# Kernel optimization log

Measured on AMD Instinct MI355X. Metric: run time of the kernel, lower is better.

Reference implementation:

```python
import jax, jax.numpy as jnp
import numpy as np

H, KD, VD = 8, 64, 64
W = 1.25  # custom weight scale


def layer_norm(x, g, b, eps=1e-5):
    m = x.mean(-1, keepdims=True)
    v = ((x - m) ** 2).mean(-1, keepdims=True)
    return (x - m) * jax.lax.rsqrt(v + eps) * g + b


def cross_attention(x1, x2, wq, wk, wv, wo, bo, wm):
    # Conv1d kernel_size=1 == matmul; channel axis splits as (heads, dim)
    b, s1, _ = x1.shape
    s2 = x2.shape[1]
    q = (x1 @ wq.T).reshape(b, s1, H, KD).transpose(0, 2, 1, 3)  # bhqk
    k = (x2 @ wk.T).reshape(b, s2, H, KD).transpose(0, 2, 1, 3)
    v = (x2 @ wv.T).reshape(b, s2, H, VD).transpose(0, 2, 1, 3)
    attn = jnp.einsum('bhqd,bhsd->bhqs', q, k) * (1.0 / (KD ** 0.5))
    attn = jax.nn.softmax(attn * wm, axis=-1)  # elementwise weight BEFORE softmax
    o = jnp.einsum('bhqs,bhsv->bhqv', attn, v)
    o = o.transpose(0, 2, 1, 3).reshape(b, s1, H * VD)
    return o @ wo.T + bo


def make_wm1(nvars, sl2, patch_num):
    sl = sl2 // 2
    wm = jnp.ones((nvars, sl2), jnp.float32)
    wm = wm.at[:2 * patch_num, :sl].multiply(W)
    wm = wm.at[2 * patch_num:, sl:].multiply(W)
    return wm[None, None]  # broadcast over batch, heads


def make_wm2(nvars, sv, patch_num, patch_num_v):
    wm = jnp.ones((nvars, sv), jnp.float32)
    wm = wm.at[:patch_num, :patch_num_v].multiply(W)
    wm = wm.at[patch_num:2 * patch_num, patch_num_v:2 * patch_num_v].multiply(W)
    wm = wm.at[2 * patch_num:, 2 * patch_num_v:].multiply(W)
    return wm[None, None]


def forward(cords_features, spatial_features, speed_features,
            wq1, wk1, wv1, wo1, bo1, wq2, wk2, wv2, wo2, bo2,
            ln1_g, ln1_b, ln2_g, ln2_b, ln3_g, ln3_b,
            ffn_w1, ffn_b1, ffn_w2, ffn_b2):
    b, nvars, d = cords_features.shape
    patch_num = nvars // 3
    patch_num_v = speed_features.shape[1] // 3
    wm1 = make_wm1(nvars, spatial_features.shape[1], patch_num)
    wm2 = make_wm2(nvars, 3 * patch_num_v, patch_num, patch_num_v)
    x = cross_attention(cords_features, spatial_features, wq1, wk1, wv1, wo1, bo1, wm1)
    x = layer_norm(x + cords_features, ln1_g, ln1_b)
    r2 = x
    x = cross_attention(x, speed_features, wq2, wk2, wv2, wo2, bo2, wm2)
    x = layer_norm(x + r2, ln2_g, ln2_b)
    r3 = x
    h = jax.nn.gelu(x @ ffn_w1.T + ffn_b1, approximate=False)
    x = h @ ffn_w2.T + ffn_b2
    return layer_norm(x + r3, ln3_g, ln3_b)


def setup_inputs():
    key = jax.random.key(0)
    ks = jax.random.split(key, 16)
    D, DF = 512, 2048
    s = 0.02
    inp = {
        'cords_features': jax.random.normal(ks[0], (8, 768, D), jnp.float32),
        'spatial_features': jax.random.normal(ks[1], (8, 1024, D), jnp.float32),
        'speed_features': jax.random.normal(ks[2], (8, 768, D), jnp.float32),
        'wq1': jax.random.normal(ks[3], (H * KD, D)) * s,
        'wk1': jax.random.normal(ks[4], (H * KD, D)) * s,
        'wv1': jax.random.normal(ks[5], (H * VD, D)) * s,
        'wo1': jax.random.normal(ks[6], (D, H * VD)) * s,
        'bo1': jnp.zeros((D,), jnp.float32),
        'wq2': jax.random.normal(ks[7], (H * KD, D)) * s,
        'wk2': jax.random.normal(ks[8], (H * KD, D)) * s,
        'wv2': jax.random.normal(ks[9], (H * VD, D)) * s,
        'wo2': jax.random.normal(ks[10], (D, H * VD)) * s,
        'bo2': jnp.zeros((D,), jnp.float32),
        'ln1_g': jnp.ones((D,), jnp.float32), 'ln1_b': jnp.zeros((D,), jnp.float32),
        'ln2_g': jnp.ones((D,), jnp.float32), 'ln2_b': jnp.zeros((D,), jnp.float32),
        'ln3_g': jnp.ones((D,), jnp.float32), 'ln3_b': jnp.zeros((D,), jnp.float32),
        'ffn_w1': jax.random.normal(ks[11], (DF, D)) * s,
        'ffn_b1': jnp.zeros((DF,), jnp.float32),
        'ffn_w2': jax.random.normal(ks[12], (D, DF)) * s,
        'ffn_b2': jnp.zeros((D,), jnp.float32),
    }
    return inp


def reference(cords_features, spatial_features, speed_features,
              wq1, wk1, wv1, wo1, bo1, wq2, wk2, wv2, wo2, bo2,
              ln1_g, ln1_b, ln2_g, ln2_b, ln3_g, ln3_b,
              ffn_w1, ffn_b1, ffn_w2, ffn_b2):
    return forward(cords_features, spatial_features, speed_features,
                   wq1, wk1, wv1, wo1, bo1, wq2, wk2, wv2, wo2, bo2,
                   ln1_g, ln1_b, ln2_g, ln2_b, ln3_g, ln3_b,
                   ffn_w1, ffn_b1, ffn_w2, ffn_b2)
```

## Files before the change

### kernel.cpp

```cpp
#include <hip/hip_runtime.h>
#include <hip/hip_bf16.h>


#define LN_EPS 1e-5f
#define WSCALE 1.25f

typedef __attribute__((ext_vector_type(8))) short short8;
typedef __attribute__((ext_vector_type(4))) float floatx4;
typedef unsigned short us;

__device__ __forceinline__ float bf2f(us u) {
    union { unsigned int i; float f; } v; v.i = ((unsigned int)u) << 16; return v.f;
}
__device__ __forceinline__ us f2bf(float f) {
    union { float f; unsigned int i; } v; v.f = f;
    return (us)((v.i + 0x7FFFu + ((v.i >> 16) & 1u)) >> 16);
}
__device__ __forceinline__ float gelu_f(float v) {
    float x  = v * 0.70710678118654752f;
    float ax = fabsf(x);
    float t  = 1.0f / (1.0f + 0.3275911f * ax);
    float p  = t * (0.254829592f + t * (-0.284496736f + t * (1.421413741f +
               t * (-1.453152027f + t * 1.061405429f))));
    float er = 1.0f - p * __expf(-ax * ax);
    er = copysignf(er, x);
    return 0.5f * v * (1.0f + er);
}

struct CastArgs {
    const float* src[13];
    us* dst[13];
    int blk_ofs[14];
};
__global__ __launch_bounds__(256) void cast_all(CastArgs a)
{
    int b = blockIdx.x;
    int e = 0;
    while (b >= a.blk_ofs[e + 1]) ++e;
    int i = ((b - a.blk_ofs[e]) * 256 + threadIdx.x) * 8;
    const float* s = a.src[e];
    us* d = a.dst[e];
    float4 x = *(const float4*)(s + i);
    float4 y = *(const float4*)(s + i + 4);
    *(ushort4*)(d + i)     = make_ushort4(f2bf(x.x), f2bf(x.y), f2bf(x.z), f2bf(x.w));
    *(ushort4*)(d + i + 4) = make_ushort4(f2bf(y.x), f2bf(y.y), f2bf(y.z), f2bf(y.w));
}

__global__ __launch_bounds__(256) void gemm64(
    const us* __restrict__ A, const us* __restrict__ Bw,
    const float* __restrict__ bias, us* __restrict__ Cb,
    int M, int N, int K, int flags)
{
    __shared__ us As[2][64 * 64];
    __shared__ us Bs[2][64 * 64];

    int t = threadIdx.x;
    int wave = t >> 6, lane = t & 63;
    int m0 = blockIdx.y * 64, n0 = blockIdx.x * 64;
    int wr = (wave >> 1) * 32, wc = (wave & 1) * 32;

    int r_in = lane >> 3;
    int pq   = lane & 7;
    const us* gA[2]; const us* gB[2];
    int lofs[2];
#pragma unroll
    for (int c = 0; c < 2; ++c) {
        int r = 16 * wave + 8 * c + r_in;
        int q = pq ^ (r & 7);
        gA[c] = A  + (size_t)(m0 + r) * K + 8 * q;
        gB[c] = Bw + (size_t)(n0 + r) * K + 8 * q;
        lofs[c] = (16 * wave + 8 * c) * 64;
    }

    int fcol = lane & 15, fj = lane >> 4;
    int aoff[2][2], boff[2][2];
#pragma unroll
    for (int mt = 0; mt < 2; ++mt)
#pragma unroll
        for (int kc = 0; kc < 2; ++kc) {
            int fr = wr + 16 * mt + fcol;
            aoff[mt][kc] = fr * 64 + ((kc * 4 + fj) ^ (fr & 7)) * 8;
            int br = wc + 16 * mt + fcol;
            boff[mt][kc] = br * 64 + ((kc * 4 + fj) ^ (br & 7)) * 8;
        }

    floatx4 acc[2][2] = {};

    auto stage = [&](int buf, int k0) {
#pragma unroll
        for (int c = 0; c < 2; ++c) {
            __builtin_amdgcn_global_load_lds(
                (const __attribute__((address_space(1))) void*)(gA[c] + k0),
                (__attribute__((address_space(3))) void*)(As[buf] + lofs[c]), 16, 0, 0);
            __builtin_amdgcn_global_load_lds(
                (const __attribute__((address_space(1))) void*)(gB[c] + k0),
                (__attribute__((address_space(3))) void*)(Bs[buf] + lofs[c]), 16, 0, 0);
        }
    };

    int ktrips = K >> 6;
    stage(0, 0);
    for (int tt = 0; tt < ktrips; ++tt) {
        int buf = tt & 1;
        if (tt + 1 < ktrips) {
            stage(buf ^ 1, (tt + 1) << 6);
            asm volatile("s_waitcnt vmcnt(4)" ::: "memory");
        } else {
            asm volatile("s_waitcnt vmcnt(0)" ::: "memory");
        }
        __builtin_amdgcn_s_barrier();
        asm volatile("" ::: "memory");

        const us* as_ = As[buf];
        const us* bs_ = Bs[buf];
        short8 af[2][2], bfr[2][2];
#pragma unroll
        for (int mt = 0; mt < 2; ++mt)
#pragma unroll
            for (int kc = 0; kc < 2; ++kc) {
                af[mt][kc]  = *(const short8*)(as_ + aoff[mt][kc]);
                bfr[mt][kc] = *(const short8*)(bs_ + boff[mt][kc]);
            }
#pragma unroll
        for (int kc = 0; kc < 2; ++kc)
#pragma unroll
            for (int mt = 0; mt < 2; ++mt)
#pragma unroll
                for (int nt = 0; nt < 2; ++nt)
                    acc[mt][nt] = __builtin_amdgcn_mfma_f32_16x16x32_bf16(
                        af[mt][kc], bfr[nt][kc], acc[mt][nt], 0, 0, 0);

        asm volatile("" ::: "memory");
        __builtin_amdgcn_s_barrier();
    }

    int rq = lane >> 4;
#pragma unroll
    for (int mt = 0; mt < 2; ++mt)
#pragma unroll
        for (int nt = 0; nt < 2; ++nt) {
            int col = n0 + wc + 16 * nt + fcol;
            float bv = (flags & 1) ? bias[col] : 0.f;
#pragma unroll
            for (int r = 0; r < 4; ++r) {
                int row = m0 + wr + 16 * mt + rq * 4 + r;
                Cb[(size_t)row * N + col] = f2bf(acc[mt][nt][r] + bv);
            }
        }
}

template<int BM, int BN>
__global__ __launch_bounds__(256) void gemm_t(
    const us* __restrict__ A, const us* __restrict__ Bw,
    const float* __restrict__ bias, float* __restrict__ Cf,
    us* __restrict__ Cb, int M, int N, int K, int flags,
    int vS, us* __restrict__ Vtg)
{
    constexpr int WN = BN / 2;
    constexpr int MT = 4;
    constexpr int NT = WN / 16;
    constexpr int CA = BM / 32;
    constexpr int CB = BN / 32;

    __shared__ us As[2][BM * 64];
    __shared__ us Bs[2][BN * 64];

    int t = threadIdx.x;
    int wave = t >> 6, lane = t & 63;
    int m0 = blockIdx.y * BM, n0 = blockIdx.x * BN;
    int wr = (wave >> 1) * 64, wc = (wave & 1) * WN;

    int r_in = lane >> 3;
    int pq   = lane & 7;
    const us* gA[CA]; int lofsA[CA];
#pragma unroll
    for (int c = 0; c < CA; ++c) {
        int r = 32 * c + 8 * wave + r_in;
        int q = pq ^ (r & 7);
        gA[c] = A + (size_t)(m0 + r) * K + 8 * q;
        lofsA[c] = (32 * c + 8 * wave) * 64;
    }
    const us* gB[CB]; int lofsB[CB];
#pragma unroll
    for (int c = 0; c < CB; ++c) {
        int r = 32 * c + 8 * wave + r_in;
        int q = pq ^ (r & 7);
        gB[c] = Bw + (size_t)(n0 + r) * K + 8 * q;
        lofsB[c] = (32 * c + 8 * wave) * 64;
    }

    int fcol = lane & 15, fj = lane >> 4;
    int aoff[MT][2], boff[NT][2];
#pragma unroll
    for (int mt = 0; mt < MT; ++mt)
#pragma unroll
        for (int kc = 0; kc < 2; ++kc) {
            int fr = wr + 16 * mt + fcol;
            aoff[mt][kc] = fr * 64 + ((kc * 4 + fj) ^ (fr & 7)) * 8;
        }
#pragma unroll
    for (int nt = 0; nt < NT; ++nt)
#pragma unroll
        for (int kc = 0; kc < 2; ++kc) {
            int br = wc + 16 * nt + fcol;
            boff[nt][kc] = br * 64 + ((kc * 4 + fj) ^ (br & 7)) * 8;
        }

    floatx4 acc[MT][NT] = {};

    auto stage = [&](int buf, int k0) {
#pragma unroll
        for (int c = 0; c < CA; ++c)
            __builtin_amdgcn_global_load_lds(
                (const __attribute__((address_space(1))) void*)(gA[c] + k0),
                (__attribute__((address_space(3))) void*)(As[buf] + lofsA[c]), 16, 0, 0);
#pragma unroll
        for (int c = 0; c < CB; ++c)
            __builtin_amdgcn_global_load_lds(
                (const __attribute__((address_space(1))) void*)(gB[c] + k0),
                (__attribute__((address_space(3))) void*)(Bs[buf] + lofsB[c]), 16, 0, 0);
    };

    int ktrips = K >> 6;
    stage(0, 0);
    for (int tt = 0; tt < ktrips; ++tt) {
        int buf = tt & 1;
        if (tt + 1 < ktrips) {
            stage(buf ^ 1, (tt + 1) << 6);
            asm volatile("s_waitcnt vmcnt(8)" ::: "memory");
        } else {
            asm volatile("s_waitcnt vmcnt(0)" ::: "memory");
        }
        __builtin_amdgcn_s_barrier();
        asm volatile("" ::: "memory");

        const us* as_ = As[buf];
        const us* bs_ = Bs[buf];
        short8 af[MT][2], bfr[NT][2];
#pragma unroll
        for (int mt = 0; mt < MT; ++mt)
#pragma unroll
            for (int kc = 0; kc < 2; ++kc)
                af[mt][kc] = *(const short8*)(as_ + aoff[mt][kc]);
#pragma unroll
        for (int nt = 0; nt < NT; ++nt)
#pragma unroll
            for (int kc = 0; kc < 2; ++kc)
                bfr[nt][kc] = *(const short8*)(bs_ + boff[nt][kc]);
#pragma unroll
        for (int kc = 0; kc < 2; ++kc)
#pragma unroll
            for (int mt = 0; mt < MT; ++mt)
#pragma unroll
                for (int nt = 0; nt < NT; ++nt)
                    acc[mt][nt] = __builtin_amdgcn_mfma_f32_16x16x32_bf16(
                        af[mt][kc], bfr[nt][kc], acc[mt][nt], 0, 0, 0);

        asm volatile("" ::: "memory");
        __builtin_amdgcn_s_barrier();
    }

    int rq = lane >> 4;
    if (flags & 8) {
        int b = m0 / vS;
        int s_base = m0 - b * vS;
        if (n0 < 512) {
#pragma unroll
            for (int mt = 0; mt < MT; ++mt)
#pragma unroll
                for (int nt = 0; nt < NT; ++nt) {
                    int col = n0 + wc + 16 * nt + fcol;
#pragma unroll
                    for (int r = 0; r < 4; ++r) {
                        int rloc = wr + 16 * mt + rq * 4 + r;
                        Cb[(size_t)(m0 + rloc) * 512 + col] = f2bf(acc[mt][nt][r]);
                    }
                }
        } else {
#pragma unroll
            for (int mt = 0; mt < MT; ++mt)
#pragma unroll
                for (int nt = 0; nt < NT; ++nt) {
                    int cv = n0 + wc + 16 * nt + fcol - 512;
                    int hv = cv >> 6, dv = cv & 63;
                    int sb = s_base + wr + 16 * mt + rq * 4;
                    ushort4 pk = make_ushort4(
                        f2bf(acc[mt][nt][0]), f2bf(acc[mt][nt][1]),
                        f2bf(acc[mt][nt][2]), f2bf(acc[mt][nt][3]));
                    *(ushort4*)(Vtg + ((size_t)(b * 8 + hv) * 64 + dv) * vS + sb) = pk;
                }
        }
        return;
    }

#pragma unroll
    for (int mt = 0; mt < MT; ++mt)
#pragma unroll
        for (int nt = 0; nt < NT; ++nt) {
            int col = n0 + wc + 16 * nt + fcol;
            float bv = (flags & 1) ? bias[col] : 0.f;
#pragma unroll
            for (int r = 0; r < 4; ++r) {
                int row = m0 + wr + 16 * mt + rq * 4 + r;
                float v = acc[mt][nt][r] + bv;
                if (flags & 2) v = gelu_f(v);
                if (flags & 4) Cb[(size_t)row * N + col] = f2bf(v);
                else           Cf[(size_t)row * N + col] = v;
            }
        }
}

__global__ __launch_bounds__(256, 3) void attn_kernel(
    const us* __restrict__ Q, const us* __restrict__ Kf,
    const us* __restrict__ Vg, us* __restrict__ O,
    int S1, int S2, int shift)
{
    __shared__ us Qs[64 * 64];
    __shared__ us Ks[2][64 * 64];
    __shared__ us Vs[2][64 * 64];
    __shared__ us Ps[64 * 72];

    int t = threadIdx.x;
    int wave = t >> 6, lane = t & 63;
    int quad = lane >> 4, l15 = lane & 15;
    int q0 = blockIdx.x * 64, hh = blockIdx.y, bb = blockIdx.z;
    int qb = wave * 16;

    int r_in = lane >> 3, pq = lane & 7;
    const us *gK[2], *gV[2];
    int lofs[2];
#pragma unroll
    for (int c2 = 0; c2 < 2; ++c2) {
        int r = qb + 8 * c2 + r_in;
        int lq = pq ^ (r & 7);
        const us* gQ = Q + ((size_t)bb * S1 + q0 + r) * 512 + hh * 64 + 8 * lq;
        gK[c2] = Kf + ((size_t)bb * S2 + r) * 512 + hh * 64 + 8 * lq;
        gV[c2] = Vg + ((size_t)(bb * 8 + hh) * 64 + r) * S2 + 8 * lq;
        lofs[c2] = (qb + 8 * c2) * 64;
        __builtin_amdgcn_global_load_lds(
            (const __attribute__((address_space(1))) void*)gQ,
            (__attribute__((address_space(3))) void*)(Qs + lofs[c2]), 16, 0, 0);
    }

    int aoffQ[2], poffP[2], boff[4][2];
#pragma unroll
    for (int kc = 0; kc < 2; ++kc) {
        int ph = ((kc * 4 + quad) ^ (l15 & 7)) * 8;
        aoffQ[kc] = (qb + l15) * 64 + ph;
        poffP[kc] = (qb + l15) * 72 + ph;
#pragma unroll
        for (int nt = 0; nt < 4; ++nt)
            boff[nt][kc] = (16 * nt + l15) * 64 + ph;
    }
    int pwoff[4][4];
#pragma unroll
    for (int r = 0; r < 4; ++r) {
        int row = qb + quad * 4 + r;
#pragma unroll
        for (int nt = 0; nt < 4; ++nt) {
            int s = 16 * nt + l15;
            pwoff[nt][r] = row * 72 + (((s >> 3) ^ (row & 7)) * 8) + (s & 7);
        }
    }

    floatx4 acc_o[4] = {};
    float l_part[4] = {0.f, 0.f, 0.f, 0.f};
    int qsh[4];
#pragma unroll
    for (int r = 0; r < 4; ++r) qsh[r] = (q0 + qb + quad * 4 + r) >> shift;

    auto stageKV = [&](int buf, int cc) {
#pragma unroll
        for (int c2 = 0; c2 < 2; ++c2) {
            __builtin_amdgcn_global_load_lds(
                (const __attribute__((address_space(1))) void*)(gK[c2] + (size_t)cc * 512),
                (__attribute__((address_space(3))) void*)(Ks[buf] + lofs[c2]), 16, 0, 0);
            __builtin_amdgcn_global_load_lds(
                (const __attribute__((address_space(1))) void*)(gV[c2] + cc),
                (__attribute__((address_space(3))) void*)(Vs[buf] + lofs[c2]), 16, 0, 0);
        }
    };

    stageKV(0, 0);
    asm volatile("s_waitcnt vmcnt(4)" ::: "memory");
    __builtin_amdgcn_s_barrier();
    asm volatile("" ::: "memory");
    short8 aq0 = *(const short8*)(Qs + aoffQ[0]);
    short8 aq1 = *(const short8*)(Qs + aoffQ[1]);

    int ntile = S2 >> 6;
    for (int ti = 0; ti < ntile; ++ti) {
        int buf = ti & 1;
        if (ti + 1 < ntile) {
            stageKV(buf ^ 1, (ti + 1) << 6);
            asm volatile("s_waitcnt vmcnt(4)" ::: "memory");
        } else {
            asm volatile("s_waitcnt vmcnt(0)" ::: "memory");
        }
        __builtin_amdgcn_s_barrier();
        asm volatile("" ::: "memory");

        const us* ks_ = Ks[buf];
        const us* vs_ = Vs[buf];
        int cbase = ti << 6;

        floatx4 s_acc[4] = {};
#pragma unroll
        for (int nt = 0; nt < 4; ++nt) {
            short8 bk0 = *(const short8*)(ks_ + boff[nt][0]);
            short8 bk1 = *(const short8*)(ks_ + boff[nt][1]);
            s_acc[nt] = __builtin_amdgcn_mfma_f32_16x16x32_bf16(aq0, bk0, s_acc[nt], 0, 0, 0);
            s_acc[nt] = __builtin_amdgcn_mfma_f32_16x16x32_bf16(aq1, bk1, s_acc[nt], 0, 0, 0);
        }

#pragma unroll
        for (int nt = 0; nt < 4; ++nt) {
            int srs = (cbase + 16 * nt + l15) >> shift;
#pragma unroll
            for (int r = 0; r < 4; ++r) {
                float fct = (qsh[r] == srs) ? (0.125f * WSCALE) : 0.125f;
                float p = __expf(s_acc[nt][r] * fct);
                s_acc[nt][r] = p;
                l_part[r] += p;
            }
        }

#pragma unroll
        for (int nt = 0; nt < 4; ++nt)
#pragma unroll
            for (int r = 0; r < 4; ++r)
                Ps[pwoff[nt][r]] = f2bf(s_acc[nt][r]);
        __builtin_amdgcn_wave_barrier();

        short8 ap0 = *(const short8*)(Ps + poffP[0]);
        short8 ap1 = *(const short8*)(Ps + poffP[1]);
#pragma unroll
        for (int nt = 0; nt < 4; ++nt) {
            short8 bv0 = *(const short8*)(vs_ + boff[nt][0]);
            short8 bv1 = *(const short8*)(vs_ + boff[nt][1]);
            acc_o[nt] = __builtin_amdgcn_mfma_f32_16x16x32_bf16(ap0, bv0, acc_o[nt], 0, 0, 0);
            acc_o[nt] = __builtin_amdgcn_mfma_f32_16x16x32_bf16(ap1, bv1, acc_o[nt], 0, 0, 0);
        }

        asm volatile("" ::: "memory");
        __builtin_amdgcn_s_barrier();
    }

#pragma unroll
    for (int r = 0; r < 4; ++r) {
#pragma unroll
        for (int off = 8; off; off >>= 1)
            l_part[r] += __shfl_xor(l_part[r], off, 16);
    }
#pragma unroll
    for (int r = 0; r < 4; ++r) {
        float inv = 1.0f / l_part[r];
        size_t base = ((size_t)bb * S1 + q0 + qb + quad * 4 + r) * 512 + hh * 64;
#pragma unroll
        for (int nt = 0; nt < 4; ++nt)
            O[base + 16 * nt + l15] = f2bf(acc_o[nt][r] * inv);
    }
}

__global__ __launch_bounds__(256) void ln_kernel(
    const us* __restrict__ X, const float* __restrict__ R,
    const float* __restrict__ g, const float* __restrict__ bta,
    float* __restrict__ out, us* __restrict__ outb)
{
    int row = blockIdx.x;
    int t   = threadIdx.x;
    const us*    xr = X + (size_t)row * 512;
    const float* rr = R + (size_t)row * 512;
    float v0 = bf2f(xr[t]) + rr[t];
    float v1 = bf2f(xr[t + 256]) + rr[t + 256];
    float s  = v0 + v1;
    float sq = v0 * v0 + v1 * v1;
#pragma unroll
    for (int off = 32; off; off >>= 1) {
        s  += __shfl_xor(s, off, 64);
        sq += __shfl_xor(sq, off, 64);
    }
    __shared__ float ps[4], psq[4];
    int w = t >> 6;
    if ((t & 63) == 0) { ps[w] = s; psq[w] = sq; }
    __syncthreads();
    float S  = ps[0] + ps[1] + ps[2] + ps[3];
    float SQ = psq[0] + psq[1] + psq[2] + psq[3];
    float mean = S * (1.0f / 512.0f);
    float var  = SQ * (1.0f / 512.0f) - mean * mean;
    float inv  = rsqrtf(var + LN_EPS);
    float y0 = (v0 - mean) * inv * g[t] + bta[t];
    float y1 = (v1 - mean) * inv * g[t + 256] + bta[t + 256];
    out[(size_t)row * 512 + t]       = y0;
    out[(size_t)row * 512 + t + 256] = y1;
    if (outb) {
        outb[(size_t)row * 512 + t]       = f2bf(y0);
        outb[(size_t)row * 512 + t + 256] = f2bf(y1);
    }
}

extern "C" void kernel_launch(void* const* d_in, const int* in_sizes, int n_in,
                              void* d_out, int out_size, void* d_ws, size_t ws_size,
                              hipStream_t stream)
{
    const float* cords   = (const float*)d_in[0];
    const float* spatial = (const float*)d_in[1];
    const float* speed   = (const float*)d_in[2];
    const float* wq1 = (const float*)d_in[3];
    const float* wk1 = (const float*)d_in[4];
    const float* wv1 = (const float*)d_in[5];
    const float* wo1 = (const float*)d_in[6];
    const float* bo1 = (const float*)d_in[7];
    const float* wq2 = (const float*)d_in[8];
    const float* wk2 = (const float*)d_in[9];
    const float* wv2 = (const float*)d_in[10];
    const float* wo2 = (const float*)d_in[11];
    const float* bo2 = (const float*)d_in[12];
    const float* ln1g = (const float*)d_in[13];
    const float* ln1b = (const float*)d_in[14];
    const float* ln2g = (const float*)d_in[15];
    const float* ln2b = (const float*)d_in[16];
    const float* ln3g = (const float*)d_in[17];
    const float* ln3b = (const float*)d_in[18];
    const float* fw1 = (const float*)d_in[19];
    const float* fb1 = (const float*)d_in[20];
    const float* fw2 = (const float*)d_in[21];
    const float* fb2 = (const float*)d_in[22];

    const int B = 8, S1 = 768, S2 = 1024, Sv = 768, D = 512, DF = 2048;
    const int M1 = B * S1;
    const int M2 = B * S2;

    char* w = (char*)d_ws;
    us* q_bf = (us*)w;              w += (size_t)M1 * D * 2;
    us* k_bf = (us*)w;              w += (size_t)M2 * D * 2;
    us* vt   = (us*)w;              w += (size_t)M2 * D * 2;
    us* o_bf = (us*)w;              w += (size_t)M1 * D * 2;
    us* p_bf = (us*)w;              w += (size_t)M1 * D * 2;
    float* x1 = (float*)w;          w += (size_t)M1 * D * 4;
    us* cords_bf   = (us*)w;        w += (size_t)M1 * D * 2;
    us* spatial_bf = (us*)w;        w += (size_t)M2 * D * 2;
    us* speed_bf   = (us*)w;        w += (size_t)M1 * D * 2;
    us* wq1b = (us*)w;              w += (size_t)D * D * 2;
    us* wk1b = (us*)w;              w += (size_t)D * D * 2;
    us* wv1b = (us*)w;              w += (size_t)D * D * 2;
    us* wo1b = (us*)w;              w += (size_t)D * D * 2;
    us* wq2b = (us*)w;              w += (size_t)D * D * 2;
    us* wk2b = (us*)w;              w += (size_t)D * D * 2;
    us* wv2b = (us*)w;              w += (size_t)D * D * 2;
    us* wo2b = (us*)w;              w += (size_t)D * D * 2;
    us* fw1b = (us*)w;              w += (size_t)DF * D * 2;
    us* fw2b = (us*)w;              w += (size_t)DF * D * 2;

    us* h_bf  = q_bf;
    us* y_bf  = p_bf;
    us* x1_bf = spatial_bf;
    us* x2_bf = cords_bf;
    float* x2 = (float*)d_out;

    dim3 blk(256);

    {
        CastArgs ca;
        const float* srcs[13] = {cords, spatial, speed, wq1, wk1, wv1, wo1,
                                 wq2, wk2, wv2, wo2, fw1, fw2};
        us* dsts[13] = {cords_bf, spatial_bf, speed_bf, wq1b, wk1b, wv1b, wo1b,
                        wq2b, wk2b, wv2b, wo2b, fw1b, fw2b};
        int ns[13] = {M1 * D, M2 * D, M1 * D, D * D, D * D, D * D, D * D,
                      D * D, D * D, D * D, D * D, DF * D, DF * D};
        int ofs = 0;
        for (int i = 0; i < 13; ++i) {
            ca.src[i] = srcs[i]; ca.dst[i] = dsts[i];
            ca.blk_ofs[i] = ofs; ofs += ns[i] / 2048;
        }
        ca.blk_ofs[13] = ofs;
        cast_all<<<dim3(ofs), blk, 0, stream>>>(ca);
    }

    auto g64  = [](int M, int N) { return dim3(N / 64,  M / 64); };
    auto g128 = [](int M, int N) { return dim3(N / 128, M / 128); };

    gemm64<<<g64(M1, D), blk, 0, stream>>>(cords_bf, wq1b, nullptr, q_bf, M1, D, D, 0);
    gemm_t<128, 128><<<g128(M2, 1024), blk, 0, stream>>>(spatial_bf, wk1b, nullptr, nullptr, k_bf,
                                                         M2, 1024, D, 8, S2, vt);
    attn_kernel<<<dim3(S1 / 64, 8, B), blk, 0, stream>>>(q_bf, k_bf, vt, o_bf, S1, S2, 9);
    gemm64<<<g64(M1, D), blk, 0, stream>>>(o_bf, wo1b, bo1, p_bf, M1, D, D, 1);
    ln_kernel<<<M1, blk, 0, stream>>>(p_bf, cords, ln1g, ln1b, x1, x1_bf);

    gemm64<<<g64(M1, D), blk, 0, stream>>>(x1_bf, wq2b, nullptr, q_bf, M1, D, D, 0);
    gemm_t<128, 128><<<g128(M1, 1024), blk, 0, stream>>>(speed_bf, wk2b, nullptr, nullptr, k_bf,
                                                         M1, 1024, D, 8, Sv, vt);
    attn_kernel<<<dim3(S1 / 64, 8, B), blk, 0, stream>>>(q_bf, k_bf, vt, o_bf, S1, Sv, 8);
    gemm64<<<g64(M1, D), blk, 0, stream>>>(o_bf, wo2b, bo2, p_bf, M1, D, D, 1);
    ln_kernel<<<M1, blk, 0, stream>>>(p_bf, x1, ln2g, ln2b, x2, x2_bf);

    gemm_t<128, 128><<<g128(M1, DF), blk, 0, stream>>>(x2_bf, fw1b, fb1, nullptr, h_bf,
                                                       M1, DF, D, 1 | 2 | 4, 0, nullptr);
    gemm64<<<g64(M1, D), blk, 0, stream>>>(h_bf, fw2b, fb2, y_bf, M1, D, DF, 1);
    ln_kernel<<<M1, blk, 0, stream>>>(y_bf, x2, ln3g, ln3b, (float*)d_out, nullptr);

    (void)in_sizes; (void)n_in; (void)out_size; (void)ws_size;
}
```

Before: 357.3 us.

## Replace double-buffered GEMM with 256x128 triple-buffer ring kernel using 512 threads

Replaces the 128x128 double-buffered gemm_t with gemm_ring. It uses 256x128 tiles, 8 waves, and a 3-slot LDS ring that prefetches two K-steps ahead. Each K-step's loads are split into two phases interleaved with the two k-chunks of MFMA work, and MFMA runs under raised s_setprio. There is one barrier per iteration instead of two. The aim is to hide global-to-LDS latency and cut barrier overhead for the K/V projections and FFN1, at the cost of more LDS per block and fewer blocks in the grid.

Result: no change. 353.7 us (-1.0%).

```diff
diff --git a/kernel.cpp b/kernel.cpp
--- a/kernel.cpp
+++ b/kernel.cpp
@@ -150,114 +150,135 @@
 }
 
 template<int BM, int BN>
-__global__ __launch_bounds__(256) void gemm_t(
+__global__ __launch_bounds__(512, 2) void gemm_ring(
     const us* __restrict__ A, const us* __restrict__ Bw,
-    const float* __restrict__ bias, float* __restrict__ Cf,
-    us* __restrict__ Cb, int M, int N, int K, int flags,
-    int vS, us* __restrict__ Vtg)
+    const float* __restrict__ bias, us* __restrict__ Cb,
+    int M, int N, int K, int flags, int vS, us* __restrict__ Vtg)
 {
-    constexpr int WN = BN / 2;
-    constexpr int MT = 4;
-    constexpr int NT = WN / 16;
-    constexpr int CA = BM / 32;
-    constexpr int CB = BN / 32;
-
-    __shared__ us As[2][BM * 64];
-    __shared__ us Bs[2][BN * 64];
+    static_assert(BM == 256 && BN == 128, "gemm_ring fixed at 256x128");
+    constexpr int SLOT = (BM + BN) * 64;
+    __shared__ us L[3 * SLOT];
 
     int t = threadIdx.x;
     int wave = t >> 6, lane = t & 63;
     int m0 = blockIdx.y * BM, n0 = blockIdx.x * BN;
-    int wr = (wave >> 1) * 64, wc = (wave & 1) * WN;
-
-    int r_in = lane >> 3;
-    int pq   = lane & 7;
-    const us* gA[CA]; int lofsA[CA];
-#pragma unroll
-    for (int c = 0; c < CA; ++c) {
-        int r = 32 * c + 8 * wave + r_in;
+    int wr = (wave >> 1) * 64, wc = (wave & 1) * 64;
+
+    int r_in = lane >> 3, pq = lane & 7;
+    const us* gA[4]; int lA[4];
+#pragma unroll
+    for (int c = 0; c < 4; ++c) {
+        int r = 64 * c + 8 * wave + r_in;
         int q = pq ^ (r & 7);
         gA[c] = A + (size_t)(m0 + r) * K + 8 * q;
-        lofsA[c] = (32 * c + 8 * wave) * 64;
-    }
-    const us* gB[CB]; int lofsB[CB];
-#pragma unroll
-    for (int c = 0; c < CB; ++c) {
-        int r = 32 * c + 8 * wave + r_in;
+        lA[c] = (64 * c + 8 * wave) * 64;
+    }
+    const us* gB[2]; int lB[2];
+#pragma unroll
+    for (int c = 0; c < 2; ++c) {
+        int r = 64 * c + 8 * wave + r_in;
         int q = pq ^ (r & 7);
         gB[c] = Bw + (size_t)(n0 + r) * K + 8 * q;
-        lofsB[c] = (32 * c + 8 * wave) * 64;
+        lB[c] = BM * 64 + (64 * c + 8 * wave) * 64;
     }
 
     int fcol = lane & 15, fj = lane >> 4;
-    int aoff[MT][2], boff[NT][2];
-#pragma unroll
-    for (int mt = 0; mt < MT; ++mt)
+    int aoff[4][2], boff[4][2];
+#pragma unroll
+    for (int mt = 0; mt < 4; ++mt)
 #pragma unroll
         for (int kc = 0; kc < 2; ++kc) {
             int fr = wr + 16 * mt + fcol;
             aoff[mt][kc] = fr * 64 + ((kc * 4 + fj) ^ (fr & 7)) * 8;
         }
 #pragma unroll
-    for (int nt = 0; nt < NT; ++nt)
+    for (int nt = 0; nt < 4; ++nt)
 #pragma unroll
         for (int kc = 0; kc < 2; ++kc) {
             int br = wc + 16 * nt + fcol;
-            boff[nt][kc] = br * 64 + ((kc * 4 + fj) ^ (br & 7)) * 8;
-        }
-
-    floatx4 acc[MT][NT] = {};
-
-    auto stage = [&](int buf, int k0) {
-#pragma unroll
-        for (int c = 0; c < CA; ++c)
+            boff[nt][kc] = BM * 64 + br * 64 + ((kc * 4 + fj) ^ (br & 7)) * 8;
+        }
+
+    floatx4 acc[4][4] = {};
+
+    auto stage_p0 = [&](int slot, int kt) {
+        us* base = L + slot * SLOT;
+#pragma unroll
+        for (int c = 0; c < 3; ++c)
             __builtin_amdgcn_global_load_lds(
-                (const __attribute__((address_space(1))) void*)(gA[c] + k0),
-                (__attribute__((address_space(3))) void*)(As[buf] + lofsA[c]), 16, 0, 0);
-#pragma unroll
-        for (int c = 0; c < CB; ++c)
+                (const __attribute__((address_space(1))) void*)(gA[c] + (size_t)kt * 64),
+                (__attribute__((address_space(3))) void*)(base + lA[c]), 16, 0, 0);
+    };
+    auto stage_p1 = [&](int slot, int kt) {
+        us* base = L + slot * SLOT;
+        __builtin_amdgcn_global_load_lds(
+            (const __attribute__((address_space(1))) void*)(gA[3] + (size_t)kt * 64),
+            (__attribute__((address_space(3))) void*)(base + lA[3]), 16, 0, 0);
+#pragma unroll
+        for (int c = 0; c < 2; ++c)
             __builtin_amdgcn_global_load_lds(
-                (const __attribute__((address_space(1))) void*)(gB[c] + k0),
-                (__attribute__((address_space(3))) void*)(Bs[buf] + lofsB[c]), 16, 0, 0);
+                (const __attribute__((address_space(1))) void*)(gB[c] + (size_t)kt * 64),
+                (__attribute__((address_space(3))) void*)(base + lB[c]), 16, 0, 0);
     };
 
     int ktrips = K >> 6;
-    stage(0, 0);
+    stage_p0(0, 0); stage_p1(0, 0);
+    if (ktrips > 1) {
+        stage_p0(1, 1); stage_p1(1, 1);
+        asm volatile("s_waitcnt vmcnt(6)" ::: "memory");
+    } else {
+        asm volatile("s_waitcnt vmcnt(0)" ::: "memory");
+    }
+    __builtin_amdgcn_s_barrier();
+    asm volatile("" ::: "memory");
+
+    int cs = 0;
     for (int tt = 0; tt < ktrips; ++tt) {
-        int buf = tt & 1;
+        int ns = cs + 2; if (ns >= 3) ns -= 3;
+        bool pre = (tt + 2) < ktrips;
+        const us* base = L + cs * SLOT;
+
+        if (pre) stage_p0(ns, tt + 2);
+        {
+            short8 af[4], bfv[4];
+#pragma unroll
+            for (int mt = 0; mt < 4; ++mt) af[mt] = *(const short8*)(base + aoff[mt][0]);
+#pragma unroll
+            for (int nt = 0; nt < 4; ++nt) bfv[nt] = *(const short8*)(base + boff[nt][0]);
+            __builtin_amdgcn_s_setprio(1);
+#pragma unroll
+            for (int mt = 0; mt < 4; ++mt)
+#pragma unroll
+                for (int nt = 0; nt < 4; ++nt)
+                    acc[mt][nt] = __builtin_amdgcn_mfma_f32_16x16x32_bf16(
+                        af[mt], bfv[nt], acc[mt][nt], 0, 0, 0);
+            __builtin_amdgcn_s_setprio(0);
+        }
+
+        if (pre) stage_p1(ns, tt + 2);
+        {
+            short8 af[4], bfv[4];
+#pragma unroll
+            for (int mt = 0; mt < 4; ++mt) af[mt] = *(const short8*)(base + aoff[mt][1]);
+#pragma unroll
+            for (int nt = 0; nt < 4; ++nt) bfv[nt] = *(const short8*)(base + boff[nt][1]);
+            __builtin_amdgcn_s_setprio(1);
+#pragma unroll
+            for (int mt = 0; mt < 4; ++mt)
+#pragma unroll
+                for (int nt = 0; nt < 4; ++nt)
+                    acc[mt][nt] = __builtin_amdgcn_mfma_f32_16x16x32_bf16(
+                        af[mt], bfv[nt], acc[mt][nt], 0, 0, 0);
+            __builtin_amdgcn_s_setprio(0);
+        }
+
         if (tt + 1 < ktrips) {
-            stage(buf ^ 1, (tt + 1) << 6);
-            asm volatile("s_waitcnt vmcnt(8)" ::: "memory");
-        } else {
-            asm volatile("s_waitcnt vmcnt(0)" ::: "memory");
-        }
-        __builtin_amdgcn_s_barrier();
-        asm volatile("" ::: "memory");
-
-        const us* as_ = As[buf];
-        const us* bs_ = Bs[buf];
-        short8 af[MT][2], bfr[NT][2];
-#pragma unroll
-        for (int mt = 0; mt < MT; ++mt)
-#pragma unroll
-            for (int kc = 0; kc < 2; ++kc)
-                af[mt][kc] = *(const short8*)(as_ + aoff[mt][kc]);
-#pragma unroll
-        for (int nt = 0; nt < NT; ++nt)
-#pragma unroll
-            for (int kc = 0; kc < 2; ++kc)
-                bfr[nt][kc] = *(const short8*)(bs_ + boff[nt][kc]);
-#pragma unroll
-        for (int kc = 0; kc < 2; ++kc)
-#pragma unroll
-            for (int mt = 0; mt < MT; ++mt)
-#pragma unroll
-                for (int nt = 0; nt < NT; ++nt)
-                    acc[mt][nt] = __builtin_amdgcn_mfma_f32_16x16x32_bf16(
-                        af[mt][kc], bfr[nt][kc], acc[mt][nt], 0, 0, 0);
-
-        asm volatile("" ::: "memory");
-        __builtin_amdgcn_s_barrier();
+            if (pre) asm volatile("s_waitcnt vmcnt(6)" ::: "memory");
+            else     asm volatile("s_waitcnt vmcnt(0)" ::: "memory");
+            __builtin_amdgcn_s_barrier();
+            asm volatile("" ::: "memory");
+        }
+        cs = cs + 1; if (cs >= 3) cs = 0;
     }
 
     int rq = lane >> 4;
@@ -266,9 +287,9 @@
         int s_base = m0 - b * vS;
         if (n0 < 512) {
 #pragma unroll
-            for (int mt = 0; mt < MT; ++mt)
-#pragma unroll
-                for (int nt = 0; nt < NT; ++nt) {
+            for (int mt = 0; mt < 4; ++mt)
+#pragma unroll
+                for (int nt = 0; nt < 4; ++nt) {
                     int col = n0 + wc + 16 * nt + fcol;
 #pragma unroll
                     for (int r = 0; r < 4; ++r) {
@@ -278,9 +299,9 @@
                 }
         } else {
 #pragma unroll
-            for (int mt = 0; mt < MT; ++mt)
-#pragma unroll
-                for (int nt = 0; nt < NT; ++nt) {
+            for (int mt = 0; mt < 4; ++mt)
+#pragma unroll
+                for (int nt = 0; nt < 4; ++nt) {
                     int cv = n0 + wc + 16 * nt + fcol - 512;
                     int hv = cv >> 6, dv = cv & 63;
                     int sb = s_base + wr + 16 * mt + rq * 4;
@@ -294,9 +315,9 @@
     }
 
 #pragma unroll
-    for (int mt = 0; mt < MT; ++mt)
-#pragma unroll
-        for (int nt = 0; nt < NT; ++nt) {
+    for (int mt = 0; mt < 4; ++mt)
+#pragma unroll
+        for (int nt = 0; nt < 4; ++nt) {
             int col = n0 + wc + 16 * nt + fcol;
             float bv = (flags & 1) ? bias[col] : 0.f;
 #pragma unroll
@@ -304,8 +325,7 @@
                 int row = m0 + wr + 16 * mt + rq * 4 + r;
                 float v = acc[mt][nt][r] + bv;
                 if (flags & 2) v = gelu_f(v);
-                if (flags & 4) Cb[(size_t)row * N + col] = f2bf(v);
-                else           Cf[(size_t)row * N + col] = v;
+                Cb[(size_t)row * N + col] = f2bf(v);
             }
         }
 }
@@ -559,6 +579,7 @@
     float* x2 = (float*)d_out;
 
     dim3 blk(256);
+    dim3 blk512(512);
 
     {
         CastArgs ca;
@@ -577,25 +598,25 @@
         cast_all<<<dim3(ofs), blk, 0, stream>>>(ca);
     }
 
-    auto g64  = [](int M, int N) { return dim3(N / 64,  M / 64); };
-    auto g128 = [](int M, int N) { return dim3(N / 128, M / 128); };
+    auto g64   = [](int M, int N) { return dim3(N / 64,  M / 64); };
+    auto gring = [](int M, int N) { return dim3(N / 128, M / 256); };
 
     gemm64<<<g64(M1, D), blk, 0, stream>>>(cords_bf, wq1b, nullptr, q_bf, M1, D, D, 0);
-    gemm_t<128, 128><<<g128(M2, 1024), blk, 0, stream>>>(spatial_bf, wk1b, nullptr, nullptr, k_bf,
-                                                         M2, 1024, D, 8, S2, vt);
+    gemm_ring<256, 128><<<gring(M2, 1024), blk512, 0, stream>>>(spatial_bf, wk1b, nullptr, k_bf,
+                                                                M2, 1024, D, 8, S2, vt);
     attn_kernel<<<dim3(S1 / 64, 8, B), blk, 0, stream>>>(q_bf, k_bf, vt, o_bf, S1, S2, 9);
     gemm64<<<g64(M1, D), blk, 0, stream>>>(o_bf, wo1b, bo1, p_bf, M1, D, D, 1);
     ln_kernel<<<M1, blk, 0, stream>>>(p_bf, cords, ln1g, ln1b, x1, x1_bf);
 
     gemm64<<<g64(M1, D), blk, 0, stream>>>(x1_bf, wq2b, nullptr, q_bf, M1, D, D, 0);
-    gemm_t<128, 128><<<g128(M1, 1024), blk, 0, stream>>>(speed_bf, wk2b, nullptr, nullptr, k_bf,
-                                                         M1, 1024, D, 8, Sv, vt);
+    gemm_ring<256, 128><<<gring(M1, 1024), blk512, 0, stream>>>(speed_bf, wk2b, nullptr, k_bf,
+                                                                M1, 1024, D, 8, Sv, vt);
     attn_kernel<<<dim3(S1 / 64, 8, B), blk, 0, stream>>>(q_bf, k_bf, vt, o_bf, S1, Sv, 8);
     gemm64<<<g64(M1, D), blk, 0, stream>>>(o_bf, wo2b, bo2, p_bf, M1, D, D, 1);
     ln_kernel<<<M1, blk, 0, stream>>>(p_bf, x1, ln2g, ln2b, x2, x2_bf);
 
-    gemm_t<128, 128><<<g128(M1, DF), blk, 0, stream>>>(x2_bf, fw1b, fb1, nullptr, h_bf,
-                                                       M1, DF, D, 1 | 2 | 4, 0, nullptr);
+    gemm_ring<256, 128><<<gring(M1, DF), blk512, 0, stream>>>(x2_bf, fw1b, fb1, h_bf,
+                                                              M1, DF, D, 1 | 2 | 4, 0, nullptr);
     gemm64<<<g64(M1, D), blk, 0, stream>>>(h_bf, fw2b, fb2, y_bf, M1, D, DF, 1);
     ln_kernel<<<M1, blk, 0, stream>>>(y_bf, x2, ln3g, ln3b, (float*)d_out, nullptr);
 
```
